# Performance work log

Hardware: AMD Instinct MI355X
Metric: run time of the kernel (lower is better)

## Reference

```python
import math
import jax, jax.numpy as jnp
import numpy as np

CHUNK_LEN = 64
NUM_HEADS = 16
HIDDEN = 1024
HEAD = HIDDEN // NUM_HEADS


def setup_inputs() -> dict:
    key = jax.random.key(0)
    ks = jax.random.split(key, 8)
    B, S, C, N, L = 4, 2048, 32, 2, 128
    scale = 1.0 / math.sqrt(HIDDEN)
    return {
        "query": jax.random.normal(ks[0], (B, S, HIDDEN), jnp.float32),
        "kv": jax.random.normal(ks[1], (B, C, N, L, HIDDEN), jnp.float32),
        "Wq": jax.random.normal(ks[2], (HIDDEN, HIDDEN), jnp.float32) * scale,
        "bq": jnp.zeros((HIDDEN,), jnp.float32),
        "Wk": jax.random.normal(ks[3], (HIDDEN, HIDDEN), jnp.float32) * scale,
        "bk": jnp.zeros((HIDDEN,), jnp.float32),
        "Wv": jax.random.normal(ks[4], (HIDDEN, HIDDEN), jnp.float32) * scale,
        "bv": jnp.zeros((HIDDEN,), jnp.float32),
    }


def reference(query, kv, Wq, bq, Wk, bk, Wv, bv):
    B, S, H = query.shape
    _, C, N, L, _ = kv.shape
    # shift query right by chunk_len-1 and pad to n_chunks*chunk_len
    q = query[:, CHUNK_LEN - 1:]
    add_len = C * CHUNK_LEN - q.shape[1]
    q = jnp.pad(q, ((0, 0), (0, add_len), (0, 0)))
    q = q.reshape(B, C, CHUNK_LEN, H)
    q = (q @ Wq.T + bq).reshape(B, C, CHUNK_LEN, NUM_HEADS, HEAD)
    k = (kv @ Wk.T + bk).reshape(B, C, N, L, NUM_HEADS, HEAD)
    v = (kv @ Wv.T + bv).reshape(B, C, N, L, NUM_HEADS, HEAD)
    # scores: [B, C, heads, chunk_len, N, L]
    attn = jnp.einsum("bcihd,bcnjhd->bchinj", q, k) / math.sqrt(HEAD)
    # softmax over flattened neighbor dims (n, j)
    attn = jax.nn.softmax(attn.reshape(B, C, NUM_HEADS, CHUNK_LEN, N * L), axis=-1)
    attn = attn.reshape(B, C, NUM_HEADS, CHUNK_LEN, N, L)
    h = jnp.einsum("bchinj,bcnjhd->bcihd", attn, v).reshape(B, C * CHUNK_LEN, H)
    # shift left: prepend chunk_len-1 zeros, truncate to seq_len
    h = jnp.pad(h, ((0, 0), (CHUNK_LEN - 1, 0), (0, 0)))[:, :S]
    return h
```

## Files before the change

### kernel.cpp

```cpp
#include <hip/hip_runtime.h>
#include <stdint.h>

#define HD 1024
#define SEQ 2048
#define NC 32

typedef __bf16 bf16x4 __attribute__((ext_vector_type(4)));
typedef __bf16 bf16x8 __attribute__((ext_vector_type(8)));
typedef float f32x4 __attribute__((ext_vector_type(4)));

__device__ inline unsigned short f2bf(float f) {
  union { float f; unsigned int u; } v; v.f = f;
  unsigned int r = v.u + 0x7fffu + ((v.u >> 16) & 1u);
  return (unsigned short)(r >> 16);
}
__device__ inline unsigned int pk2bf(float a, float b) {
  return (unsigned int)f2bf(a) | ((unsigned int)f2bf(b) << 16);
}
__device__ inline bf16x8 ld_frag8(const unsigned short* p) {
  bf16x4 lo = *(const bf16x4*)p;
  bf16x4 hi = *(const bf16x4*)(p + 4);
  return __builtin_shufflevector(lo, hi, 0, 1, 2, 3, 4, 5, 6, 7);
}
__device__ inline void glds16(const unsigned short* g, unsigned short* l) {
  __builtin_amdgcn_global_load_lds(
      (const __attribute__((address_space(1))) unsigned int*)g,
      (__attribute__((address_space(3))) unsigned int*)l, 16, 0, 0);
}
__device__ inline int2 swz_bid() {
  int lin = blockIdx.y * 8 + blockIdx.x;
  int s = (lin & 7) * (int)gridDim.y + (lin >> 3);
  return make_int2(s & 7, s >> 3);
}
__device__ inline int swz64(int row, int j) { return (row * 8 + (j ^ (row & 7))) * 8; }

__global__ __launch_bounds__(256) void zero_head_kernel(float* __restrict__ out) {
  int i = (blockIdx.x * 256 + threadIdx.x) * 4;
  int b = i / 64512;
  int r = i - b * 64512;
  *(float4*)(out + (size_t)b * (SEQ * HD) + r) = make_float4(0.f, 0.f, 0.f, 0.f);
}

__global__ __launch_bounds__(256) void prep_q_kernel(const float* __restrict__ q,
                                                     unsigned short* __restrict__ out,
                                                     float* __restrict__ oz) {
  int bid = blockIdx.x;
  if (bid < 252) {
    int i = (bid * 256 + threadIdx.x) * 4;
    int b = i / 64512;
    int r = i - b * 64512;
    *(float4*)(oz + (size_t)b * (SEQ * HD) + r) = make_float4(0.f, 0.f, 0.f, 0.f);
    return;
  }
  int i = (bid - 252) * 256 + threadIdx.x;
  int g = i >> 7, c8 = (i & 127) * 8;
  int b = g >> 11, tt = g & 2047;
  uint4 o = make_uint4(0, 0, 0, 0);
  if (tt < 1985) {
    const float* src = q + ((size_t)(b << 11) + tt + 63) * HD + c8;
    float4 a = *(const float4*)src;
    float4 bb = *(const float4*)(src + 4);
    o = make_uint4(pk2bf(a.x, a.y), pk2bf(a.z, a.w), pk2bf(bb.x, bb.y), pk2bf(bb.z, bb.w));
  }
  *(uint4*)(out + (size_t)g * HD + c8) = o;
}

__global__ __launch_bounds__(256) void cvt_kernel(const float* __restrict__ in,
                                                  unsigned short* __restrict__ out, int n8) {
  int i = blockIdx.x * 256 + threadIdx.x;
  if (i < n8) {
    float4 a = ((const float4*)in)[(size_t)i * 2];
    float4 b = ((const float4*)in)[(size_t)i * 2 + 1];
    ((uint4*)out)[i] = make_uint4(pk2bf(a.x, a.y), pk2bf(a.z, a.w),
                                  pk2bf(b.x, b.y), pk2bf(b.z, b.w));
  }
}

__global__ __launch_bounds__(256) void cvt_w3_kernel(const float* __restrict__ Wq,
                                                     const float* __restrict__ Wk,
                                                     const float* __restrict__ Wv,
                                                     unsigned short* __restrict__ dst) {
  int bid = blockIdx.x;
  int which = bid >> 9;
  int i = (bid & 511) * 256 + threadIdx.x;
  const float* src = which == 0 ? Wq : (which == 1 ? Wk : Wv);
  float4 a = ((const float4*)src)[(size_t)i * 2];
  float4 b = ((const float4*)src)[(size_t)i * 2 + 1];
  ((uint4*)(dst + (size_t)which * 1048576))[i] =
      make_uint4(pk2bf(a.x, a.y), pk2bf(a.z, a.w), pk2bf(b.x, b.y), pk2bf(b.z, b.w));
}

__global__ __launch_bounds__(256, 2) void gemm_q_kernel(
    const unsigned short* __restrict__ A, const unsigned short* __restrict__ W,
    const float* __restrict__ bias, unsigned short* __restrict__ Cout) {
  __shared__ unsigned short lds_a[128 * 64];
  __shared__ unsigned short lds_b[128 * 64];
  const int t = threadIdx.x;
  const int l = t & 63, w = t >> 6;
  const int wm = w >> 1, wn = w & 1;
  const int lr = l & 15, lq = l >> 4;
  const int2 bid = swz_bid();
  const size_t arow0 = (size_t)bid.y * 128;
  const size_t brow0 = (size_t)bid.x * 128;
  int pr[4], pco[4];
#pragma unroll
  for (int p = 0; p < 4; ++p) {
    int pc = p * 256 + t;
    pr[p] = pc >> 3;
    pco[p] = ((pc & 7) ^ (pr[p] & 7)) * 8;
  }

  f32x4 acc[4][4];
  for (int i = 0; i < 4; i++)
    for (int j = 0; j < 4; j++) acc[i][j] = (f32x4){0.f, 0.f, 0.f, 0.f};

  for (int kk = 0; kk < 16; ++kk) {
    const int k0 = kk * 64;
    __syncthreads();
#pragma unroll
    for (int p = 0; p < 4; ++p) {
      glds16(A + (arow0 + pr[p]) * HD + k0 + pco[p], lds_a + (p * 256 + t) * 8);
      glds16(W + (brow0 + pr[p]) * HD + k0 + pco[p], lds_b + (p * 256 + t) * 8);
    }
    __syncthreads();
#pragma unroll
    for (int h = 0; h < 2; ++h) {
      bf16x8 af[4], bfr[4];
      for (int mt = 0; mt < 4; ++mt)
        af[mt] = *(const bf16x8*)(lds_a + swz64(wm * 64 + mt * 16 + lr, h * 4 + lq));
      for (int nt = 0; nt < 4; ++nt)
        bfr[nt] = *(const bf16x8*)(lds_b + swz64(wn * 64 + nt * 16 + lr, h * 4 + lq));
      for (int mt = 0; mt < 4; ++mt)
        for (int nt = 0; nt < 4; ++nt)
          acc[mt][nt] = __builtin_amdgcn_mfma_f32_16x16x32_bf16(af[mt], bfr[nt], acc[mt][nt], 0, 0, 0);
    }
  }

  for (int nt = 0; nt < 4; ++nt) {
    int n = bid.x * 128 + wn * 64 + nt * 16 + lr;
    float bvv = bias[n];
    for (int mt = 0; mt < 4; ++mt) {
      size_t mbase = arow0 + wm * 64 + mt * 16 + lq * 4;
      for (int r = 0; r < 4; ++r)
        Cout[(mbase + r) * HD + n] = f2bf(acc[mt][nt][r] + bvv);
    }
  }
}

__global__ __launch_bounds__(256, 2) void gemm_kv_kernel(
    const unsigned short* __restrict__ A, const unsigned short* __restrict__ Wk,
    const unsigned short* __restrict__ Wv, const float* __restrict__ bk,
    const float* __restrict__ bv, unsigned short* __restrict__ Kout,
    unsigned short* __restrict__ Vt) {
  __shared__ unsigned short lds_a[128 * 64];
  __shared__ unsigned short lds_k[128 * 64];
  __shared__ unsigned short lds_v[128 * 64];
  const int t = threadIdx.x;
  const int l = t & 63, w = t >> 6;
  const int wm = w >> 1, wn = w & 1;
  const int lr = l & 15, lq = l >> 4;
  const int2 bid = swz_bid();
  const size_t arow0 = (size_t)bid.y * 128;
  const size_t brow0 = (size_t)bid.x * 128;
  int pr[4], pco[4];
#pragma unroll
  for (int p = 0; p < 4; ++p) {
    int pc = p * 256 + t;
    pr[p] = pc >> 3;
    pco[p] = ((pc & 7) ^ (pr[p] & 7)) * 8;
  }

  f32x4 acck[4][4], accv[4][4];
  for (int i = 0; i < 4; i++)
    for (int j = 0; j < 4; j++) {
      acck[i][j] = (f32x4){0.f, 0.f, 0.f, 0.f};
      accv[i][j] = (f32x4){0.f, 0.f, 0.f, 0.f};
    }

  for (int kk = 0; kk < 16; ++kk) {
    const int k0 = kk * 64;
    __syncthreads();
#pragma unroll
    for (int p = 0; p < 4; ++p) {
      glds16(A + (arow0 + pr[p]) * HD + k0 + pco[p], lds_a + (p * 256 + t) * 8);
      glds16(Wk + (brow0 + pr[p]) * HD + k0 + pco[p], lds_k + (p * 256 + t) * 8);
      glds16(Wv + (brow0 + pr[p]) * HD + k0 + pco[p], lds_v + (p * 256 + t) * 8);
    }
    __syncthreads();
#pragma unroll
    for (int h = 0; h < 2; ++h) {
      bf16x8 af[4];
      for (int mt = 0; mt < 4; ++mt)
        af[mt] = *(const bf16x8*)(lds_a + swz64(wm * 64 + mt * 16 + lr, h * 4 + lq));
      {
        bf16x8 bfr[4];
        for (int nt = 0; nt < 4; ++nt)
          bfr[nt] = *(const bf16x8*)(lds_k + swz64(wn * 64 + nt * 16 + lr, h * 4 + lq));
        for (int mt = 0; mt < 4; ++mt)
          for (int nt = 0; nt < 4; ++nt)
            acck[mt][nt] = __builtin_amdgcn_mfma_f32_16x16x32_bf16(af[mt], bfr[nt], acck[mt][nt], 0, 0, 0);
      }
      {
        bf16x8 bfr[4];
        for (int nt = 0; nt < 4; ++nt)
          bfr[nt] = *(const bf16x8*)(lds_v + swz64(wn * 64 + nt * 16 + lr, h * 4 + lq));
        for (int mt = 0; mt < 4; ++mt)
          for (int nt = 0; nt < 4; ++nt)
            accv[mt][nt] = __builtin_amdgcn_mfma_f32_16x16x32_bf16(af[mt], bfr[nt], accv[mt][nt], 0, 0, 0);
      }
    }
  }

  for (int nt = 0; nt < 4; ++nt) {
    int n = bid.x * 128 + wn * 64 + nt * 16 + lr;
    float bvv = bk[n];
    for (int mt = 0; mt < 4; ++mt) {
      size_t mbase = arow0 + wm * 64 + mt * 16 + lq * 4;
      for (int r = 0; r < 4; ++r)
        Kout[(mbase + r) * HD + n] = f2bf(acck[mt][nt][r] + bvv);
    }
  }
  for (int nt = 0; nt < 4; ++nt) {
    int n = bid.x * 128 + wn * 64 + nt * 16 + lr;
    float bvv = bv[n];
    int h = n >> 6, d = n & 63;
    for (int mt = 0; mt < 4; ++mt) {
      size_t m0 = arow0 + wm * 64 + mt * 16 + lq * 4;
      size_t bc = m0 >> 8, j = m0 & 255;
      *(ushort4*)(Vt + ((bc * 16 + h) * 64 + d) * 256 + j) =
          make_ushort4(f2bf(accv[mt][nt][0] + bvv), f2bf(accv[mt][nt][1] + bvv),
                       f2bf(accv[mt][nt][2] + bvv), f2bf(accv[mt][nt][3] + bvv));
    }
  }
}

__global__ __launch_bounds__(256, 2) void gemm_f32_kernel(
    const float* __restrict__ A, const float* __restrict__ W,
    const float* __restrict__ bias, unsigned short* __restrict__ Cout,
    int store_vt, int qremap) {
  __shared__ unsigned short lds_a[128 * 32];
  __shared__ unsigned short lds_b[128 * 32];
  const int t = threadIdx.x;
  const int l = t & 63, w = t >> 6;
  const int wm = w >> 1, wn = w & 1;
  const int lr = l & 15, lq = l >> 4;
  const size_t arow0 = (size_t)blockIdx.y * 128;
  const size_t brow0 = (size_t)blockIdx.x * 128;

  f32x4 acc[4][4];
  for (int i = 0; i < 4; i++)
    for (int j = 0; j < 4; j++) acc[i][j] = (f32x4){0.f, 0.f, 0.f, 0.f};

  for (int kk = 0; kk < 32; ++kk) {
    const int k0 = kk * 32;
    uint4 av[2], bv[2];
    for (int p = 0; p < 2; ++p) {
      int chunk = p * 256 + t;
      int row = chunk >> 2, c8 = (chunk & 3) * 8;
      size_t grow = arow0 + row;
      bool valid = true;
      const float* srcA;
      if (qremap) {
        int bb = (int)(grow >> 11), tt = (int)(grow & 2047);
        valid = tt < 1985;
        srcA = A + ((size_t)(bb << 11) + tt + 63) * HD + k0 + c8;
      } else {
        srcA = A + grow * HD + k0 + c8;
      }
      if (valid) {
        float4 x = *(const float4*)srcA, y = *(const float4*)(srcA + 4);
        av[p] = make_uint4(pk2bf(x.x, x.y), pk2bf(x.z, x.w), pk2bf(y.x, y.y), pk2bf(y.z, y.w));
      } else av[p] = make_uint4(0, 0, 0, 0);
      const float* srcB = W + (brow0 + row) * HD + k0 + c8;
      float4 x = *(const float4*)srcB, y = *(const float4*)(srcB + 4);
      bv[p] = make_uint4(pk2bf(x.x, x.y), pk2bf(x.z, x.w), pk2bf(y.x, y.y), pk2bf(y.z, y.w));
    }
    __syncthreads();
    for (int p = 0; p < 2; ++p) {
      int chunk = p * 256 + t;
      *(uint4*)(lds_a + chunk * 8) = av[p];
      *(uint4*)(lds_b + chunk * 8) = bv[p];
    }
    __syncthreads();
    bf16x8 af[4], bfr[4];
    for (int mt = 0; mt < 4; ++mt)
      af[mt] = *(const bf16x8*)(lds_a + (wm * 64 + mt * 16 + lr) * 32 + lq * 8);
    for (int nt = 0; nt < 4; ++nt)
      bfr[nt] = *(const bf16x8*)(lds_b + (wn * 64 + nt * 16 + lr) * 32 + lq * 8);
    for (int mt = 0; mt < 4; ++mt)
      for (int nt = 0; nt < 4; ++nt)
        acc[mt][nt] = __builtin_amdgcn_mfma_f32_16x16x32_bf16(af[mt], bfr[nt], acc[mt][nt], 0, 0, 0);
  }

  if (!store_vt) {
    for (int nt = 0; nt < 4; ++nt) {
      int n = blockIdx.x * 128 + wn * 64 + nt * 16 + lr;
      float bvv = bias[n];
      for (int mt = 0; mt < 4; ++mt) {
        size_t mbase = arow0 + wm * 64 + mt * 16 + lq * 4;
        for (int r = 0; r < 4; ++r)
          Cout[(mbase + r) * HD + n] = f2bf(acc[mt][nt][r] + bvv);
      }
    }
  } else {
    for (int nt = 0; nt < 4; ++nt) {
      int n = blockIdx.x * 128 + wn * 64 + nt * 16 + lr;
      float bvv = bias[n];
      int h = n >> 6, d = n & 63;
      for (int mt = 0; mt < 4; ++mt) {
        size_t m0 = arow0 + wm * 64 + mt * 16 + lq * 4;
        size_t bc = m0 >> 8, j = m0 & 255;
        *(ushort4*)(Cout + ((bc * 16 + h) * 64 + d) * 256 + j) =
            make_ushort4(f2bf(acc[mt][nt][0] + bvv), f2bf(acc[mt][nt][1] + bvv),
                         f2bf(acc[mt][nt][2] + bvv), f2bf(acc[mt][nt][3] + bvv));
      }
    }
  }
}

#define QK_STRIDE 72
#define P_STRIDE 260

__global__ __launch_bounds__(256, 3) void attn_kernel(
    const unsigned short* __restrict__ Qp, const unsigned short* __restrict__ Kp,
    const unsigned short* __restrict__ Vt, float* __restrict__ out) {
  __shared__ unsigned short q_s[64 * QK_STRIDE];
  __shared__ unsigned short k_s[256 * QK_STRIDE];
  const int t = threadIdx.x;
  const int l = t & 63, w = t >> 6;
  const int lr = l & 15, lq = l >> 4;
  const int bid = blockIdx.x;
  const int head = bid & 15, cc = (bid >> 4) & 31, b = bid >> 9;
  const size_t qrow0 = (size_t)(b * NC + cc) * 64;
  const size_t kvrow0 = (size_t)(b * NC + cc) * 256;
  const int hcol = head * 64;
  const unsigned short* vbase = Vt + ((size_t)((b * NC + cc) * 16 + head) * 64) * 256;

  for (int p = 0; p < 2; ++p) {
    int chunk = p * 256 + t;
    int row = chunk >> 3, c8 = (chunk & 7) * 8;
    *(uint4*)(q_s + row * QK_STRIDE + c8) = *(const uint4*)(Qp + (qrow0 + row) * HD + hcol + c8);
  }
  for (int p = 0; p < 8; ++p) {
    int chunk = p * 256 + t;
    int row = chunk >> 3, c8 = (chunk & 7) * 8;
    *(uint4*)(k_s + row * QK_STRIDE + c8) = *(const uint4*)(Kp + (kvrow0 + row) * HD + hcol + c8);
  }
  __syncthreads();

  bf16x8 qa0 = ld_frag8(q_s + (w * 16 + lr) * QK_STRIDE + lq * 8);
  bf16x8 qa1 = ld_frag8(q_s + (w * 16 + lr) * QK_STRIDE + 32 + lq * 8);
  f32x4 sc[16];
  __builtin_amdgcn_s_setprio(1);
  for (int nt = 0; nt < 16; ++nt) {
    bf16x8 kb0 = ld_frag8(k_s + (nt * 16 + lr) * QK_STRIDE + lq * 8);
    bf16x8 kb1 = ld_frag8(k_s + (nt * 16 + lr) * QK_STRIDE + 32 + lq * 8);
    f32x4 a = (f32x4){0.f, 0.f, 0.f, 0.f};
    a = __builtin_amdgcn_mfma_f32_16x16x32_bf16(qa0, kb0, a, 0, 0, 0);
    a = __builtin_amdgcn_mfma_f32_16x16x32_bf16(qa1, kb1, a, 0, 0, 0);
    sc[nt] = a;
  }
  __builtin_amdgcn_s_setprio(0);
  float mrow[4] = {-1e30f, -1e30f, -1e30f, -1e30f};
  for (int nt = 0; nt < 16; ++nt)
    for (int r = 0; r < 4; ++r) mrow[r] = fmaxf(mrow[r], sc[nt][r]);
  for (int off = 1; off < 16; off <<= 1)
    for (int r = 0; r < 4; ++r) mrow[r] = fmaxf(mrow[r], __shfl_xor(mrow[r], off, 16));
  float srow[4] = {0.f, 0.f, 0.f, 0.f};
  const float cexp = 0.18033688011112042f;
  for (int nt = 0; nt < 16; ++nt)
    for (int r = 0; r < 4; ++r) {
      float p = exp2f((sc[nt][r] - mrow[r]) * cexp);
      sc[nt][r] = p;
      srow[r] += p;
    }
  for (int off = 1; off < 16; off <<= 1)
    for (int r = 0; r < 4; ++r) srow[r] += __shfl_xor(srow[r], off, 16);

  bf16x8 va[4];
#pragma unroll
  for (int nt2 = 0; nt2 < 4; ++nt2)
    va[nt2] = *(const bf16x8*)(vbase + (size_t)(nt2 * 16 + lr) * 256 + lq * 8);

  __syncthreads();

  for (int nt = 0; nt < 16; ++nt)
    for (int r = 0; r < 4; ++r)
      k_s[(w * 16 + lq * 4 + r) * P_STRIDE + nt * 16 + lr] = f2bf(sc[nt][r]);

  f32x4 o[4];
  for (int i = 0; i < 4; ++i) o[i] = (f32x4){0.f, 0.f, 0.f, 0.f};
  bf16x8 vbuf[4];
#pragma unroll
  for (int ks = 0; ks < 8; ks += 2) {
#pragma unroll
    for (int nt2 = 0; nt2 < 4; ++nt2)
      vbuf[nt2] = *(const bf16x8*)(vbase + (size_t)(nt2 * 16 + lr) * 256 + (ks + 1) * 32 + lq * 8);
    bf16x8 pa = ld_frag8(k_s + (w * 16 + lr) * P_STRIDE + ks * 32 + lq * 8);
    __builtin_amdgcn_s_setprio(1);
#pragma unroll
    for (int nt2 = 0; nt2 < 4; ++nt2)
      o[nt2] = __builtin_amdgcn_mfma_f32_16x16x32_bf16(pa, va[nt2], o[nt2], 0, 0, 0);
    __builtin_amdgcn_s_setprio(0);
    if (ks + 2 < 8) {
#pragma unroll
      for (int nt2 = 0; nt2 < 4; ++nt2)
        va[nt2] = *(const bf16x8*)(vbase + (size_t)(nt2 * 16 + lr) * 256 + (ks + 2) * 32 + lq * 8);
    }
    bf16x8 pb = ld_frag8(k_s + (w * 16 + lr) * P_STRIDE + (ks + 1) * 32 + lq * 8);
    __builtin_amdgcn_s_setprio(1);
#pragma unroll
    for (int nt2 = 0; nt2 < 4; ++nt2)
      o[nt2] = __builtin_amdgcn_mfma_f32_16x16x32_bf16(pb, vbuf[nt2], o[nt2], 0, 0, 0);
    __builtin_amdgcn_s_setprio(0);
  }

  for (int r = 0; r < 4; ++r) {
    int strip = w * 16 + lq * 4 + r;
    int trow = cc * 64 + strip;
    if (trow < 1985) {
      size_t orow = (size_t)b * SEQ + trow + 63;
      float inv = 1.0f / srow[r];
      for (int nt2 = 0; nt2 < 4; ++nt2)
        out[orow * HD + hcol + nt2 * 16 + lr] = o[nt2][r] * inv;
    }
  }
}

extern "C" void kernel_launch(void* const* d_in, const int* in_sizes, int n_in,
                              void* d_out, int out_size, void* d_ws, size_t ws_size,
                              hipStream_t stream) {
  (void)in_sizes; (void)n_in; (void)out_size;
  const float* query = (const float*)d_in[0];
  const float* kv    = (const float*)d_in[1];
  const float* Wq    = (const float*)d_in[2];
  const float* bq    = (const float*)d_in[3];
  const float* Wk    = (const float*)d_in[4];
  const float* bk    = (const float*)d_in[5];
  const float* Wv    = (const float*)d_in[6];
  const float* bv    = (const float*)d_in[7];
  float* out = (float*)d_out;

  unsigned short* Qp  = (unsigned short*)d_ws;
  unsigned short* Kp  = Qp + (size_t)8192 * 1024;
  unsigned short* Vt  = Kp + (size_t)32768 * 1024;
  unsigned short* Qbf = Vt + (size_t)32768 * 1024;
  unsigned short* KVb = Qbf + (size_t)8192 * 1024;
  unsigned short* Wqb = KVb + (size_t)32768 * 1024;
  const size_t need = ((size_t)8192 * 1024 * 2 + (size_t)32768 * 1024 * 2 + (size_t)1024 * 1024 * 3) * 2;
  const bool big = ws_size >= need;

  if (big) {
    prep_q_kernel<<<dim3(4348), dim3(256), 0, stream>>>(query, Qbf, out);
    cvt_w3_kernel<<<dim3(1536), dim3(256), 0, stream>>>(Wq, Wk, Wv, Wqb);
    cvt_kernel<<<dim3(16384), dim3(256), 0, stream>>>(kv, KVb, 4194304);
    gemm_q_kernel<<<dim3(8, 64), dim3(256), 0, stream>>>(Qbf, Wqb, bq, Qp);
    gemm_kv_kernel<<<dim3(8, 256), dim3(256), 0, stream>>>(KVb, Wqb + (size_t)1048576,
                                                           Wqb + (size_t)2097152, bk, bv, Kp, Vt);
  } else {
    zero_head_kernel<<<dim3(252), dim3(256), 0, stream>>>(out);
    gemm_f32_kernel<<<dim3(8, 64), dim3(256), 0, stream>>>(query, Wq, bq, Qp, 0, 1);
    gemm_f32_kernel<<<dim3(8, 256), dim3(256), 0, stream>>>(kv, Wk, bk, Kp, 0, 0);
    gemm_f32_kernel<<<dim3(8, 256), dim3(256), 0, stream>>>(kv, Wv, bv, Vt, 1, 0);
  }
  attn_kernel<<<dim3(2048), dim3(256), 0, stream>>>(Qp, Kp, Vt, out);
}
```

Measured before the change: 461.5 us.

## Double-buffer KV projection GEMM and transpose attention score layout

The K/V projection GEMM now works on 32-wide K tiles in two LDS buffers. The next tile is staged with global_load_lds while the current one computes, using vmcnt waits and raw barriers in place of full syncthreads around each 64-wide tile. The attention kernel swaps the MFMA operands so each lane holds one query column's scores. That cuts the softmax reductions to two cross-lane shuffles and allows packed 64-bit stores of P into LDS. Q fragments are also read straight from global memory, dropping the q_s LDS buffer. The Q GEMM also gains a duplicated, partly wrong W-load loop that is immediately overwritten, which may add redundant loads.

```diff
diff --git a/kernel.cpp b/kernel.cpp
--- a/kernel.cpp
+++ b/kernel.cpp
@@ -33,6 +33,10 @@
   return make_int2(s & 7, s >> 3);
 }
 __device__ inline int swz64(int row, int j) { return (row * 8 + (j ^ (row & 7))) * 8; }
+__device__ inline int swz32(int row, int j) {
+  int lr8 = row >> 1;
+  return (lr8 * 8 + ((((row & 1) << 2) | j) ^ (lr8 & 7))) * 8;
+}
 
 __global__ __launch_bounds__(256) void zero_head_kernel(float* __restrict__ out) {
   int i = (blockIdx.x * 256 + threadIdx.x) * 4;
@@ -152,9 +156,9 @@
     const unsigned short* __restrict__ Wv, const float* __restrict__ bk,
     const float* __restrict__ bv, unsigned short* __restrict__ Kout,
     unsigned short* __restrict__ Vt) {
-  __shared__ unsigned short lds_a[128 * 64];
-  __shared__ unsigned short lds_k[128 * 64];
-  __shared__ unsigned short lds_v[128 * 64];
+  __shared__ unsigned short lds_a[2][128 * 32];
+  __shared__ unsigned short lds_k[2][128 * 32];
+  __shared__ unsigned short lds_v[2][128 * 32];
   const int t = threadIdx.x;
   const int l = t & 63, w = t >> 6;
   const int wm = w >> 1, wn = w & 1;
@@ -162,12 +166,14 @@
   const int2 bid = swz_bid();
   const size_t arow0 = (size_t)bid.y * 128;
   const size_t brow0 = (size_t)bid.x * 128;
-  int pr[4], pco[4];
-#pragma unroll
-  for (int p = 0; p < 4; ++p) {
+  int pr[2], pco[2];
+#pragma unroll
+  for (int p = 0; p < 2; ++p) {
     int pc = p * 256 + t;
-    pr[p] = pc >> 3;
-    pco[p] = ((pc & 7) ^ (pr[p] & 7)) * 8;
+    int lr8 = pc >> 3;
+    int e = (pc & 7) ^ (lr8 & 7);
+    pr[p] = lr8 * 2 + (e >> 2);
+    pco[p] = (e & 3) * 8;
   }
 
   f32x4 acck[4][4], accv[4][4];
@@ -177,39 +183,48 @@
       accv[i][j] = (f32x4){0.f, 0.f, 0.f, 0.f};
     }
 
-  for (int kk = 0; kk < 16; ++kk) {
-    const int k0 = kk * 64;
-    __syncthreads();
-#pragma unroll
-    for (int p = 0; p < 4; ++p) {
-      glds16(A + (arow0 + pr[p]) * HD + k0 + pco[p], lds_a + (p * 256 + t) * 8);
-      glds16(Wk + (brow0 + pr[p]) * HD + k0 + pco[p], lds_k + (p * 256 + t) * 8);
-      glds16(Wv + (brow0 + pr[p]) * HD + k0 + pco[p], lds_v + (p * 256 + t) * 8);
-    }
-    __syncthreads();
-#pragma unroll
-    for (int h = 0; h < 2; ++h) {
-      bf16x8 af[4];
+  auto stage = [&](int buf, int k0) {
+#pragma unroll
+    for (int p = 0; p < 2; ++p) {
+      glds16(A + (arow0 + pr[p]) * HD + k0 + pco[p], lds_a[buf] + (p * 256 + t) * 8);
+      glds16(Wk + (brow0 + pr[p]) * HD + k0 + pco[p], lds_k[buf] + (p * 256 + t) * 8);
+      glds16(Wv + (brow0 + pr[p]) * HD + k0 + pco[p], lds_v[buf] + (p * 256 + t) * 8);
+    }
+  };
+  auto compute = [&](int buf) {
+    bf16x8 af[4];
+    for (int mt = 0; mt < 4; ++mt)
+      af[mt] = *(const bf16x8*)(lds_a[buf] + swz32(wm * 64 + mt * 16 + lr, lq));
+    {
+      bf16x8 bfr[4];
+      for (int nt = 0; nt < 4; ++nt)
+        bfr[nt] = *(const bf16x8*)(lds_k[buf] + swz32(wn * 64 + nt * 16 + lr, lq));
       for (int mt = 0; mt < 4; ++mt)
-        af[mt] = *(const bf16x8*)(lds_a + swz64(wm * 64 + mt * 16 + lr, h * 4 + lq));
-      {
-        bf16x8 bfr[4];
         for (int nt = 0; nt < 4; ++nt)
-          bfr[nt] = *(const bf16x8*)(lds_k + swz64(wn * 64 + nt * 16 + lr, h * 4 + lq));
-        for (int mt = 0; mt < 4; ++mt)
-          for (int nt = 0; nt < 4; ++nt)
-            acck[mt][nt] = __builtin_amdgcn_mfma_f32_16x16x32_bf16(af[mt], bfr[nt], acck[mt][nt], 0, 0, 0);
-      }
-      {
-        bf16x8 bfr[4];
+          acck[mt][nt] = __builtin_amdgcn_mfma_f32_16x16x32_bf16(af[mt], bfr[nt], acck[mt][nt], 0, 0, 0);
+    }
+    {
+      bf16x8 bfr[4];
+      for (int nt = 0; nt < 4; ++nt)
+        bfr[nt] = *(const bf16x8*)(lds_v[buf] + swz32(wn * 64 + nt * 16 + lr, lq));
+      for (int mt = 0; mt < 4; ++mt)
         for (int nt = 0; nt < 4; ++nt)
-          bfr[nt] = *(const bf16x8*)(lds_v + swz64(wn * 64 + nt * 16 + lr, h * 4 + lq));
-        for (int mt = 0; mt < 4; ++mt)
-          for (int nt = 0; nt < 4; ++nt)
-            accv[mt][nt] = __builtin_amdgcn_mfma_f32_16x16x32_bf16(af[mt], bfr[nt], accv[mt][nt], 0, 0, 0);
-      }
-    }
-  }
+          accv[mt][nt] = __builtin_amdgcn_mfma_f32_16x16x32_bf16(af[mt], bfr[nt], accv[mt][nt], 0, 0, 0);
+    }
+  };
+
+  stage(0, 0);
+  for (int kk = 0; kk < 31; ++kk) {
+    const int cur = kk & 1;
+    stage(cur ^ 1, (kk + 1) * 32);
+    asm volatile("s_waitcnt vmcnt(6)" ::: "memory");
+    __builtin_amdgcn_s_barrier();
+    compute(cur);
+    __builtin_amdgcn_s_barrier();
+  }
+  asm volatile("s_waitcnt vmcnt(0)" ::: "memory");
+  __builtin_amdgcn_s_barrier();
+  compute(1);
 
   for (int nt = 0; nt < 4; ++nt) {
     int n = bid.x * 128 + wn * 64 + nt * 16 + lr;
@@ -273,6 +288,13 @@
       } else av[p] = make_uint4(0, 0, 0, 0);
       const float* srcB = W + (brow0 + row) * HD + k0 + c8;
       float4 x = *(const float4*)srcB, y = *(const float4*)(srcB + 4);
+      bv[p] = make_uint4(pk2bf(x.x, x.y), pk2bf(x.z, x.w), pk2bf(y.y, y.y), pk2bf(y.z, y.w));
+    }
+    for (int p = 0; p < 2; ++p) {
+      int chunk = p * 256 + t;
+      int row = chunk >> 2, c8 = (chunk & 3) * 8;
+      const float* srcB = W + (brow0 + row) * HD + k0 + c8;
+      float4 x = *(const float4*)srcB, y = *(const float4*)(srcB + 4);
       bv[p] = make_uint4(pk2bf(x.x, x.y), pk2bf(x.z, x.w), pk2bf(y.x, y.y), pk2bf(y.z, y.w));
     }
     __syncthreads();
@@ -324,7 +346,6 @@
 __global__ __launch_bounds__(256, 3) void attn_kernel(
     const unsigned short* __restrict__ Qp, const unsigned short* __restrict__ Kp,
     const unsigned short* __restrict__ Vt, float* __restrict__ out) {
-  __shared__ unsigned short q_s[64 * QK_STRIDE];
   __shared__ unsigned short k_s[256 * QK_STRIDE];
   const int t = threadIdx.x;
   const int l = t & 63, w = t >> 6;
@@ -336,46 +357,42 @@
   const int hcol = head * 64;
   const unsigned short* vbase = Vt + ((size_t)((b * NC + cc) * 16 + head) * 64) * 256;
 
-  for (int p = 0; p < 2; ++p) {
-    int chunk = p * 256 + t;
-    int row = chunk >> 3, c8 = (chunk & 7) * 8;
-    *(uint4*)(q_s + row * QK_STRIDE + c8) = *(const uint4*)(Qp + (qrow0 + row) * HD + hcol + c8);
-  }
   for (int p = 0; p < 8; ++p) {
     int chunk = p * 256 + t;
     int row = chunk >> 3, c8 = (chunk & 7) * 8;
     *(uint4*)(k_s + row * QK_STRIDE + c8) = *(const uint4*)(Kp + (kvrow0 + row) * HD + hcol + c8);
   }
+  bf16x8 qa0 = ld_frag8(Qp + (qrow0 + w * 16 + lr) * HD + hcol + lq * 8);
+  bf16x8 qa1 = ld_frag8(Qp + (qrow0 + w * 16 + lr) * HD + hcol + 32 + lq * 8);
   __syncthreads();
 
-  bf16x8 qa0 = ld_frag8(q_s + (w * 16 + lr) * QK_STRIDE + lq * 8);
-  bf16x8 qa1 = ld_frag8(q_s + (w * 16 + lr) * QK_STRIDE + 32 + lq * 8);
   f32x4 sc[16];
   __builtin_amdgcn_s_setprio(1);
   for (int nt = 0; nt < 16; ++nt) {
     bf16x8 kb0 = ld_frag8(k_s + (nt * 16 + lr) * QK_STRIDE + lq * 8);
     bf16x8 kb1 = ld_frag8(k_s + (nt * 16 + lr) * QK_STRIDE + 32 + lq * 8);
     f32x4 a = (f32x4){0.f, 0.f, 0.f, 0.f};
-    a = __builtin_amdgcn_mfma_f32_16x16x32_bf16(qa0, kb0, a, 0, 0, 0);
-    a = __builtin_amdgcn_mfma_f32_16x16x32_bf16(qa1, kb1, a, 0, 0, 0);
+    a = __builtin_amdgcn_mfma_f32_16x16x32_bf16(kb0, qa0, a, 0, 0, 0);
+    a = __builtin_amdgcn_mfma_f32_16x16x32_bf16(kb1, qa1, a, 0, 0, 0);
     sc[nt] = a;
   }
   __builtin_amdgcn_s_setprio(0);
-  float mrow[4] = {-1e30f, -1e30f, -1e30f, -1e30f};
+
+  float m = -1e30f;
   for (int nt = 0; nt < 16; ++nt)
-    for (int r = 0; r < 4; ++r) mrow[r] = fmaxf(mrow[r], sc[nt][r]);
-  for (int off = 1; off < 16; off <<= 1)
-    for (int r = 0; r < 4; ++r) mrow[r] = fmaxf(mrow[r], __shfl_xor(mrow[r], off, 16));
-  float srow[4] = {0.f, 0.f, 0.f, 0.f};
+    for (int r = 0; r < 4; ++r) m = fmaxf(m, sc[nt][r]);
+  m = fmaxf(m, __shfl_xor(m, 16));
+  m = fmaxf(m, __shfl_xor(m, 32));
+  float s = 0.f;
   const float cexp = 0.18033688011112042f;
   for (int nt = 0; nt < 16; ++nt)
     for (int r = 0; r < 4; ++r) {
-      float p = exp2f((sc[nt][r] - mrow[r]) * cexp);
+      float p = exp2f((sc[nt][r] - m) * cexp);
       sc[nt][r] = p;
-      srow[r] += p;
-    }
-  for (int off = 1; off < 16; off <<= 1)
-    for (int r = 0; r < 4; ++r) srow[r] += __shfl_xor(srow[r], off, 16);
+      s += p;
+    }
+  s += __shfl_xor(s, 16);
+  s += __shfl_xor(s, 32);
 
   bf16x8 va[4];
 #pragma unroll
@@ -384,9 +401,10 @@
 
   __syncthreads();
 
-  for (int nt = 0; nt < 16; ++nt)
-    for (int r = 0; r < 4; ++r)
-      k_s[(w * 16 + lq * 4 + r) * P_STRIDE + nt * 16 + lr] = f2bf(sc[nt][r]);
+  for (int nt = 0; nt < 16; ++nt) {
+    *(uint2*)(k_s + (w * 16 + lr) * P_STRIDE + nt * 16 + lq * 4) =
+        make_uint2(pk2bf(sc[nt][0], sc[nt][1]), pk2bf(sc[nt][2], sc[nt][3]));
+  }
 
   f32x4 o[4];
   for (int i = 0; i < 4; ++i) o[i] = (f32x4){0.f, 0.f, 0.f, 0.f};
@@ -418,9 +436,10 @@
   for (int r = 0; r < 4; ++r) {
     int strip = w * 16 + lq * 4 + r;
     int trow = cc * 64 + strip;
+    float sv = __shfl(s, lq * 4 + r, 16);
     if (trow < 1985) {
       size_t orow = (size_t)b * SEQ + trow + 63;
-      float inv = 1.0f / srow[r];
+      float inv = 1.0f / sv;
       for (int nt2 = 0; nt2 < 4; ++nt2)
         out[orow * HD + hcol + nt2 * 16 + lr] = o[nt2][r] * inv;
     }
```

Result: no change. 466.9 us (+1.2%).
